# Kernel tuning notes

Measured on AMD Instinct MI355X. Metric: run time of the kernel, lower is better.

## Reference

```python
import math
import jax, jax.numpy as jnp
import numpy as np

B, N, C = 64, 197, 768
H = 12
D = C // H
SCALE = D ** -0.5
EPS_SM = 1e-6
LN_EPS = 1e-5


def _layernorm(x, w, b):
    mu = jnp.mean(x, axis=-1, keepdims=True)
    var = jnp.var(x, axis=-1, keepdims=True)
    return (x - mu) * jax.lax.rsqrt(var + LN_EPS) * w + b


def setup_inputs() -> dict:
    key = jax.random.key(0)
    ks = jax.random.split(key, 12)
    s = 0.02
    return {
        "x": jax.random.normal(ks[0], (B, N, C), jnp.float32),
        "mask": jnp.ones((B, N), jnp.float32),
        "ln1_w": jnp.ones((C,), jnp.float32),
        "ln1_b": jnp.zeros((C,), jnp.float32),
        "qkv_w": jax.random.normal(ks[1], (C, 3 * C), jnp.float32) * s,
        "qkv_b": jnp.zeros((3 * C,), jnp.float32),
        "proj_w": jax.random.normal(ks[2], (C, C), jnp.float32) * s,
        "proj_b": jnp.zeros((C,), jnp.float32),
        "ln2_w": jnp.ones((C,), jnp.float32),
        "ln2_b": jnp.zeros((C,), jnp.float32),
        "fc1_w": jax.random.normal(ks[3], (C, 4 * C), jnp.float32) * s,
        "fc1_b": jnp.zeros((4 * C,), jnp.float32),
        "fc2_w": jax.random.normal(ks[4], (4 * C, C), jnp.float32) * s,
        "fc2_b": jnp.zeros((C,), jnp.float32),
        "threshold": jnp.float32(0.0),
    }


def reference(x, mask, ln1_w, ln1_b, qkv_w, qkv_b, proj_w, proj_b,
              ln2_w, ln2_b, fc1_w, fc1_b, fc2_w, fc2_b, threshold):
    # --- LTPAttention ---
    h = _layernorm(x, ln1_w, ln1_b)
    qkv = (h @ qkv_w + qkv_b).reshape(B, N, 3, H, D)
    qkv = jnp.transpose(qkv, (2, 0, 3, 1, 4))  # (3, B, H, N, D)
    q, k, v = qkv[0], qkv[1], qkv[2]
    attn = jnp.einsum("bhnd,bhmd->bhnm", q, k) * SCALE  # (B,H,N,N)
    # softmax_with_mask (eval path): exp * key-mask, renormalize
    m = mask[:, None, None, :]  # (B,1,1,N) masks keys
    w = jnp.exp(attn - jnp.max(attn, axis=-1, keepdims=True)) * m
    attn = w / (jnp.sum(w, axis=-1, keepdims=True) + EPS_SM)
    out = jnp.einsum("bhnm,bhmd->bhnd", attn, v)
    out = jnp.transpose(out, (0, 2, 1, 3)).reshape(B, N, C)
    x_attn = out @ proj_w + proj_b
    # importance scores: mean over heads and queries -> (B, N)
    imp = jnp.mean(attn, axis=(1, 2))
    imp = imp.at[:, 0].set(jnp.inf)  # always keep CLS token
    # ThresholdMasker (eval): hard threshold
    new_mask = (imp > threshold).astype(mask.dtype)
    mask_out = jnp.where(mask > 0, new_mask, mask)
    # --- residual + MLP ---
    x = x + x_attn
    h2 = _layernorm(x, ln2_w, ln2_b)
    h2 = jax.nn.gelu(h2 @ fc1_w + fc1_b, approximate=False)
    x = x + (h2 @ fc2_w + fc2_b)
    return x, mask_out
```

## Files before the change

### kernel.cpp

```cpp
#include <hip/hip_runtime.h>
#include <hip/hip_bf16.h>
#include <math.h>

#define B_ 64
#define N_ 197
#define C_ 768
#define H_ 12
#define BN_ (B_ * N_)
#define MPAD 12672
#define GRIDM 99

typedef unsigned short ushort_t;
typedef __attribute__((ext_vector_type(8))) short short8;
typedef __attribute__((ext_vector_type(4))) float f32x4;

__device__ __forceinline__ float wave_reduce_sum(float v) {
#pragma unroll
  for (int off = 32; off; off >>= 1) v += __shfl_xor(v, off);
  return v;
}

__device__ __forceinline__ ushort_t f2bf(float f) {
  __hip_bfloat16 h = __float2bfloat16(f);
  ushort_t u;
  __builtin_memcpy(&u, &h, 2);
  return u;
}

__device__ __forceinline__ float gelu_fast(float u) {
  const float z2 = 1.5957691216f * (u + 0.044715f * u * u * u);
  const float e = __expf(z2);
  const float th = 1.f - 2.f / (e + 1.f);
  return 0.5f * u * (1.f + th);
}

__global__ __launch_bounds__(256) void wtrans_kernel(const float* __restrict__ W,
                                                     ushort_t* __restrict__ Wt,
                                                     int K, int N) {
  __shared__ ushort_t tile[32][33];
  const int bn = blockIdx.x * 32, bk = blockIdx.y * 32;
  const int tx = threadIdx.x & 31, ty = threadIdx.x >> 5;
#pragma unroll
  for (int i = ty; i < 32; i += 8)
    tile[i][tx] = f2bf(W[(size_t)(bk + i) * N + bn + tx]);
  __syncthreads();
#pragma unroll
  for (int i = ty; i < 32; i += 8)
    Wt[(size_t)(bn + i) * K + bk + tx] = tile[tx][i];
}

__global__ __launch_bounds__(256) void ln_kernel(const float* __restrict__ x,
                                                 const float* __restrict__ w,
                                                 const float* __restrict__ bsh,
                                                 ushort_t* __restrict__ out) {
  const int row = blockIdx.x;
  const float* xr = x + (size_t)row * C_;
  const int tid = threadIdx.x;
  float v0 = xr[tid], v1 = xr[tid + 256], v2 = xr[tid + 512];
  float s = v0 + v1 + v2;
  float q = v0 * v0 + v1 * v1 + v2 * v2;
  s = wave_reduce_sum(s);
  q = wave_reduce_sum(q);
  __shared__ float red[8];
  const int w4 = tid >> 6, l = tid & 63;
  if (l == 0) { red[w4] = s; red[4 + w4] = q; }
  __syncthreads();
  float ts = red[0] + red[1] + red[2] + red[3];
  float tq = red[4] + red[5] + red[6] + red[7];
  float mu = ts * (1.f / C_);
  float var = tq * (1.f / C_) - mu * mu;
  float rs = rsqrtf(var + 1e-5f);
  ushort_t* orow = out + (size_t)row * C_;
  orow[tid]       = f2bf((v0 - mu) * rs * w[tid]       + bsh[tid]);
  orow[tid + 256] = f2bf((v1 - mu) * rs * w[tid + 256] + bsh[tid + 256]);
  orow[tid + 512] = f2bf((v2 - mu) * rs * w[tid + 512] + bsh[tid + 512]);
}

template <int RES, int ACT, int OUT_BF16>
__global__ __launch_bounds__(256) void mfma_gemm(const ushort_t* __restrict__ A,
                                                 const ushort_t* __restrict__ Bt,
                                                 const float* __restrict__ bias,
                                                 const float* __restrict__ res,
                                                 void* __restrict__ Cout,
                                                 int M, int Nc, int K, int gridN) {
  __shared__ __align__(16) ushort_t As0[128][32];
  __shared__ __align__(16) ushort_t As1[128][32];
  __shared__ __align__(16) ushort_t As2[128][32];
  __shared__ __align__(16) ushort_t As3[128][32];
  __shared__ __align__(16) ushort_t Bs0[128][32];
  __shared__ __align__(16) ushort_t Bs1[128][32];
  __shared__ __align__(16) ushort_t Bs2[128][32];
  __shared__ __align__(16) ushort_t Bs3[128][32];

  const int flat = blockIdx.x;
  const int x8 = flat & 7, q8 = flat >> 3;
  const int n_t = q8 % gridN, jj = q8 / gridN;
  const int m_t = jj * 8 + x8;
  if (m_t >= GRIDM) return;

  const int tid = threadIdx.x;
  const int w = tid >> 6, l = tid & 63;
  const int bm = m_t * 128, bnn = n_t * 128;
  const int quad = l >> 4, lm = l & 15;
  const int wm = (w >> 1) * 64, wn = (w & 1) * 64;

  const int c0 = w * 2, c1 = w * 2 + 1;
  const int srow = l >> 2;
  const int scol = ((l & 3) ^ ((l >> 3) & 3)) << 3;
  const ushort_t* ag0 = A + (size_t)(bm + c0 * 16 + srow) * K + scol;
  const ushort_t* ag1 = A + (size_t)(bm + c1 * 16 + srow) * K + scol;
  const ushort_t* bg0 = Bt + (size_t)(bnn + c0 * 16 + srow) * K + scol;
  const ushort_t* bg1 = Bt + (size_t)(bnn + c1 * 16 + srow) * K + scol;

  auto stage = [&](ushort_t (*Ad)[32], ushort_t (*Bd)[32], int k0) {
    __builtin_amdgcn_global_load_lds(
        (const __attribute__((address_space(1))) void*)(ag0 + k0),
        (__attribute__((address_space(3))) void*)&Ad[c0 * 16][0], 16, 0, 0);
    __builtin_amdgcn_global_load_lds(
        (const __attribute__((address_space(1))) void*)(ag1 + k0),
        (__attribute__((address_space(3))) void*)&Ad[c1 * 16][0], 16, 0, 0);
    __builtin_amdgcn_global_load_lds(
        (const __attribute__((address_space(1))) void*)(bg0 + k0),
        (__attribute__((address_space(3))) void*)&Bd[c0 * 16][0], 16, 0, 0);
    __builtin_amdgcn_global_load_lds(
        (const __attribute__((address_space(1))) void*)(bg1 + k0),
        (__attribute__((address_space(3))) void*)&Bd[c1 * 16][0], 16, 0, 0);
  };

  const int fslot = (quad ^ ((lm >> 1) & 3)) << 3;

  f32x4 acc[4][4];
#pragma unroll
  for (int mi = 0; mi < 4; mi++)
#pragma unroll
    for (int ni = 0; ni < 4; ni++) acc[mi][ni] = (f32x4){0.f, 0.f, 0.f, 0.f};

  const int NIT = K >> 5;

#define GSTEP(Ac, Bc, An, Bn, tn, VMN, DOSTAGE)                         \
  {                                                                     \
    asm volatile("s_waitcnt vmcnt(" #VMN ")" ::: "memory");             \
    __builtin_amdgcn_s_barrier();                                       \
    asm volatile("" ::: "memory");                                      \
    if (DOSTAGE) stage(An, Bn, (tn) << 5);                              \
    short8 af[4], bf[4];                                                \
    _Pragma("unroll") for (int i = 0; i < 4; i++) {                     \
      af[i] = *(const short8*)&Ac[wm + i * 16 + lm][fslot];             \
      bf[i] = *(const short8*)&Bc[wn + i * 16 + lm][fslot];             \
    }                                                                   \
    _Pragma("unroll") for (int mi = 0; mi < 4; mi++)                    \
      _Pragma("unroll") for (int ni = 0; ni < 4; ni++)                  \
        acc[mi][ni] = __builtin_amdgcn_mfma_f32_16x16x32_bf16(          \
            af[mi], bf[ni], acc[mi][ni], 0, 0, 0);                      \
  }

  stage(As0, Bs0, 0);
  stage(As1, Bs1, 1 << 5);
  stage(As2, Bs2, 2 << 5);
  int t = 0;
  for (; t < NIT - 4; t += 4) {
    GSTEP(As0, Bs0, As3, Bs3, t + 3, 8, true);
    GSTEP(As1, Bs1, As0, Bs0, t + 4, 8, true);
    GSTEP(As2, Bs2, As1, Bs1, t + 5, 8, true);
    GSTEP(As3, Bs3, As2, Bs2, t + 6, 8, true);
  }
  GSTEP(As0, Bs0, As3, Bs3, t + 3, 8, true);
  GSTEP(As1, Bs1, As0, Bs0, 0, 8, false);
  GSTEP(As2, Bs2, As0, Bs0, 0, 4, false);
  GSTEP(As3, Bs3, As0, Bs0, 0, 0, false);
#undef GSTEP

#pragma unroll
  for (int mi = 0; mi < 4; mi++) {
#pragma unroll
    for (int ni = 0; ni < 4; ni++) {
      const int col = bnn + wn + ni * 16 + lm;
      const float bv = bias[col];
#pragma unroll
      for (int r = 0; r < 4; r++) {
        const int row = bm + wm + mi * 16 + quad * 4 + r;
        if (row < M) {
          float v = acc[mi][ni][r] + bv;
          if constexpr (RES) v += res[(size_t)row * Nc + col];
          if constexpr (ACT) v = gelu_fast(v);
          if constexpr (OUT_BF16)
            ((ushort_t*)Cout)[(size_t)row * Nc + col] = f2bf(v);
          else
            ((float*)Cout)[(size_t)row * Nc + col] = v;
        }
      }
    }
  }
}

__global__ __launch_bounds__(256, 2) void attn_mfma(const ushort_t* __restrict__ qkv,
                                                    const float* __restrict__ mask,
                                                    ushort_t* __restrict__ aout,
                                                    float* __restrict__ imp) {
  __shared__ __align__(16) ushort_t Ks[208 * 64];
  __shared__ __align__(16) ushort_t Vt[64 * 216];
  __shared__ __align__(16) ushort_t Pb[4][16 * 208];
  const int b = blockIdx.x / H_, h = blockIdx.x % H_;
  const int tid = threadIdx.x, w = tid >> 6, l = tid & 63;
  const int quad = l >> 4, lm = l & 15;
  const ushort_t* qbase = qkv + (size_t)b * N_ * 2304 + h * 64;
  const ushort_t* kbase = qbase + 768;
  const ushort_t* vbase = qbase + 1536;

  for (int idx = tid; idx < 208 * 8; idx += 256) {
    const int j = idx >> 3, g = idx & 7;
    uint4 val = make_uint4(0u, 0u, 0u, 0u);
    if (j < N_) val = *(const uint4*)(kbase + (size_t)j * 2304 + g * 8);
    *(uint4*)&Ks[j * 64 + ((g ^ (j & 7)) << 3)] = val;
  }
  for (int idx = tid; idx < 52 * 64; idx += 256) {
    const int d = idx & 63, jg = idx >> 6, j0 = jg * 4;
    ushort_t a0 = 0, a1 = 0, a2 = 0, a3 = 0;
    if (j0 + 0 < N_) a0 = vbase[(size_t)(j0 + 0) * 2304 + d];
    if (j0 + 1 < N_) a1 = vbase[(size_t)(j0 + 1) * 2304 + d];
    if (j0 + 2 < N_) a2 = vbase[(size_t)(j0 + 2) * 2304 + d];
    if (j0 + 3 < N_) a3 = vbase[(size_t)(j0 + 3) * 2304 + d];
    uint2 pk;
    pk.x = (unsigned)a0 | ((unsigned)a1 << 16);
    pk.y = (unsigned)a2 | ((unsigned)a3 << 16);
    *(uint2*)&Vt[d * 216 + j0] = pk;
  }
  float mkv[13];
#pragma unroll
  for (int t = 0; t < 13; t++) {
    const int col = t * 16 + lm;
    mkv[t] = (col < N_) ? mask[b * N_ + col] : 0.f;
  }
  float cs[13];
#pragma unroll
  for (int t = 0; t < 13; t++) cs[t] = 0.f;
  __syncthreads();

  ushort_t* pw = &Pb[w][0];
  for (int i0 = w * 16; i0 < 208; i0 += 64) {
    f32x4 accs[13];
#pragma unroll
    for (int t = 0; t < 13; t++) accs[t] = (f32x4){0.f, 0.f, 0.f, 0.f};
#pragma unroll
    for (int kh = 0; kh < 2; kh++) {
      const int k0 = kh * 32;
      const short8 aq =
          *(const short8*)(qbase + (size_t)(i0 + lm) * 2304 + k0 + quad * 8);
      const int gb = (k0 >> 3) + quad;
#pragma unroll
      for (int t = 0; t < 13; t++) {
        const int j = t * 16 + lm;
        const short8 bk = *(const short8*)&Ks[j * 64 + ((gb ^ (j & 7)) << 3)];
        accs[t] = __builtin_amdgcn_mfma_f32_16x16x32_bf16(aq, bk, accs[t], 0, 0, 0);
      }
    }
    float inv[4];
#pragma unroll
    for (int r = 0; r < 4; r++) {
      float m = -3.4e38f;
#pragma unroll
      for (int t = 0; t < 13; t++) m = fmaxf(m, accs[t][r] * 0.125f);
      m = fmaxf(m, __shfl_xor(m, 1));
      m = fmaxf(m, __shfl_xor(m, 2));
      m = fmaxf(m, __shfl_xor(m, 4));
      m = fmaxf(m, __shfl_xor(m, 8));
      float s = 0.f;
#pragma unroll
      for (int t = 0; t < 13; t++) {
        const float e = __expf(accs[t][r] * 0.125f - m) * mkv[t];
        accs[t][r] = e;
        s += e;
      }
      s += __shfl_xor(s, 1);
      s += __shfl_xor(s, 2);
      s += __shfl_xor(s, 4);
      s += __shfl_xor(s, 8);
      inv[r] = 1.f / (s + 1e-6f);
    }
    const int ibase = i0 + quad * 4;
#pragma unroll
    for (int r = 0; r < 4; r++) {
      const bool rok = (ibase + r) < N_;
#pragma unroll
      for (int t = 0; t < 13; t++) {
        const float p = accs[t][r] * inv[r];
        accs[t][r] = p;
        if (rok) cs[t] += p;
        pw[(quad * 4 + r) * 208 + t * 16 + lm] = f2bf(p);
      }
    }
    __builtin_amdgcn_wave_barrier();
    f32x4 acco[4];
#pragma unroll
    for (int n = 0; n < 4; n++) acco[n] = (f32x4){0.f, 0.f, 0.f, 0.f};
#pragma unroll
    for (int ks = 0; ks < 6; ks++) {
      const int k0 = ks * 32;
      const short8 ap = *(const short8*)&pw[lm * 208 + k0 + quad * 8];
#pragma unroll
      for (int n = 0; n < 4; n++) {
        const short8 bv = *(const short8*)&Vt[(n * 16 + lm) * 216 + k0 + quad * 8];
        acco[n] = __builtin_amdgcn_mfma_f32_16x16x32_bf16(ap, bv, acco[n], 0, 0, 0);
      }
    }
    {
      const bool lo = (quad < 2);
      short8 apt = {};
      if (lo) apt = *(const short8*)&pw[lm * 208 + 192 + quad * 8];
#pragma unroll
      for (int n = 0; n < 4; n++) {
        short8 bvt = {};
        if (lo) bvt = *(const short8*)&Vt[(n * 16 + lm) * 216 + 192 + quad * 8];
        acco[n] = __builtin_amdgcn_mfma_f32_16x16x32_bf16(apt, bvt, acco[n], 0, 0, 0);
      }
    }
#pragma unroll
    for (int r = 0; r < 4; r++) {
      const int i = ibase + r;
      if (i < N_) {
#pragma unroll
        for (int n = 0; n < 4; n++)
          aout[(size_t)(b * N_ + i) * C_ + h * 64 + n * 16 + lm] = f2bf(acco[n][r]);
      }
    }
  }
#pragma unroll
  for (int t = 0; t < 13; t++) {
    float v = cs[t];
    v += __shfl_xor(v, 16);
    v += __shfl_xor(v, 32);
    if (l < 16) {
      const int col = t * 16 + l;
      if (col < N_)
        atomicAdd(&imp[b * N_ + col], v * (1.f / (H_ * (float)N_)));
    }
  }
}

__global__ __launch_bounds__(256) void mask_kernel(const float* __restrict__ imp,
                                                   const float* __restrict__ mask,
                                                   const float* __restrict__ thr,
                                                   float* __restrict__ mask_out) {
  const int i = blockIdx.x * 256 + threadIdx.x;
  if (i >= BN_) return;
  const int n = i % N_;
  const float iv = (n == 0) ? INFINITY : imp[i];
  const float m = mask[i];
  const float nm = (iv > thr[0]) ? 1.f : 0.f;
  mask_out[i] = (m > 0.f) ? nm : m;
}

extern "C" void kernel_launch(void* const* d_in, const int* in_sizes, int n_in,
                              void* d_out, int out_size, void* d_ws, size_t ws_size,
                              hipStream_t stream) {
  const float* x      = (const float*)d_in[0];
  const float* mask   = (const float*)d_in[1];
  const float* ln1_w  = (const float*)d_in[2];
  const float* ln1_b  = (const float*)d_in[3];
  const float* qkv_w  = (const float*)d_in[4];
  const float* qkv_b  = (const float*)d_in[5];
  const float* proj_w = (const float*)d_in[6];
  const float* proj_b = (const float*)d_in[7];
  const float* ln2_w  = (const float*)d_in[8];
  const float* ln2_b  = (const float*)d_in[9];
  const float* fc1_w  = (const float*)d_in[10];
  const float* fc1_b  = (const float*)d_in[11];
  const float* fc2_w  = (const float*)d_in[12];
  const float* fc2_b  = (const float*)d_in[13];
  const float* thr    = (const float*)d_in[14];

  float* out = (float*)d_out;
  float* mask_out = out + (size_t)BN_ * C_;

  ushort_t* buf0    = (ushort_t*)d_ws;
  ushort_t* hbuf    = buf0 + (size_t)MPAD * 3072;
  ushort_t* aoutb   = hbuf + (size_t)MPAD * 768;
  ushort_t* qkv_wt  = aoutb + (size_t)MPAD * 768;
  ushort_t* proj_wt = qkv_wt + (size_t)2304 * 768;
  ushort_t* fc1_wt  = proj_wt + (size_t)768 * 768;
  ushort_t* fc2_wt  = fc1_wt + (size_t)3072 * 768;
  float*    impb    = (float*)(fc2_wt + (size_t)768 * 3072);

  hipMemsetAsync(impb, 0, BN_ * sizeof(float), stream);

  wtrans_kernel<<<dim3(2304 / 32, 768 / 32), 256, 0, stream>>>(qkv_w, qkv_wt, 768, 2304);
  wtrans_kernel<<<dim3(768 / 32, 768 / 32), 256, 0, stream>>>(proj_w, proj_wt, 768, 768);
  wtrans_kernel<<<dim3(3072 / 32, 768 / 32), 256, 0, stream>>>(fc1_w, fc1_wt, 768, 3072);
  wtrans_kernel<<<dim3(768 / 32, 3072 / 32), 256, 0, stream>>>(fc2_w, fc2_wt, 3072, 768);

  const int MS = 13 * 8;
  ln_kernel<<<BN_, 256, 0, stream>>>(x, ln1_w, ln1_b, hbuf);
  mfma_gemm<0, 0, 1><<<MS * 18, 256, 0, stream>>>(
      hbuf, qkv_wt, qkv_b, nullptr, buf0, BN_, 2304, 768, 18);
  attn_mfma<<<B_ * H_, 256, 0, stream>>>(buf0, mask, aoutb, impb);
  mask_kernel<<<(BN_ + 255) / 256, 256, 0, stream>>>(impb, mask, thr, mask_out);
  mfma_gemm<1, 0, 0><<<MS * 6, 256, 0, stream>>>(
      aoutb, proj_wt, proj_b, x, out, BN_, 768, 768, 6);
  ln_kernel<<<BN_, 256, 0, stream>>>(out, ln2_w, ln2_b, hbuf);
  mfma_gemm<0, 1, 1><<<MS * 24, 256, 0, stream>>>(
      hbuf, fc1_wt, fc1_b, nullptr, buf0, BN_, 3072, 768, 24);
  mfma_gemm<1, 0, 0><<<MS * 6, 256, 0, stream>>>(
      buf0, fc2_wt, fc2_b, out, out, BN_, 768, 3072, 6);
}
```

Measured before the change: 603.3 us.

## Replace four-stage BK=32 GEMM ring with double-buffered BK=64 pipeline

Restructures the MFMA GEMM main loop from a four-slot ring of 32-wide K tiles, which uses fine-grained vmcnt waits, into a two-buffer scheme. Each buffer holds a 64-wide K tile split into two 32-column halves, and full __syncthreads separate the stages. The aim is fewer barriers per K element and simpler control flow. In exchange, prefetch depth drops to one tile ahead and each barrier waits for all outstanding loads, so memory latency may be hidden less well. The loop also assumes K/64 is even.

```diff
diff --git a/kernel.cpp b/kernel.cpp
--- a/kernel.cpp
+++ b/kernel.cpp
@@ -83,14 +83,14 @@
                                                  const float* __restrict__ res,
                                                  void* __restrict__ Cout,
                                                  int M, int Nc, int K, int gridN) {
-  __shared__ __align__(16) ushort_t As0[128][32];
-  __shared__ __align__(16) ushort_t As1[128][32];
-  __shared__ __align__(16) ushort_t As2[128][32];
-  __shared__ __align__(16) ushort_t As3[128][32];
-  __shared__ __align__(16) ushort_t Bs0[128][32];
-  __shared__ __align__(16) ushort_t Bs1[128][32];
-  __shared__ __align__(16) ushort_t Bs2[128][32];
-  __shared__ __align__(16) ushort_t Bs3[128][32];
+  __shared__ __align__(16) ushort_t As0h0[128][32];
+  __shared__ __align__(16) ushort_t As0h1[128][32];
+  __shared__ __align__(16) ushort_t As1h0[128][32];
+  __shared__ __align__(16) ushort_t As1h1[128][32];
+  __shared__ __align__(16) ushort_t Bs0h0[128][32];
+  __shared__ __align__(16) ushort_t Bs0h1[128][32];
+  __shared__ __align__(16) ushort_t Bs1h0[128][32];
+  __shared__ __align__(16) ushort_t Bs1h1[128][32];
 
   const int flat = blockIdx.x;
   const int x8 = flat & 7, q8 = flat >> 3;
@@ -112,7 +112,7 @@
   const ushort_t* bg0 = Bt + (size_t)(bnn + c0 * 16 + srow) * K + scol;
   const ushort_t* bg1 = Bt + (size_t)(bnn + c1 * 16 + srow) * K + scol;
 
-  auto stage = [&](ushort_t (*Ad)[32], ushort_t (*Bd)[32], int k0) {
+  auto stage_h = [&](ushort_t (*Ad)[32], ushort_t (*Bd)[32], int k0) {
     __builtin_amdgcn_global_load_lds(
         (const __attribute__((address_space(1))) void*)(ag0 + k0),
         (__attribute__((address_space(3))) void*)&Ad[c0 * 16][0], 16, 0, 0);
@@ -135,14 +135,8 @@
 #pragma unroll
     for (int ni = 0; ni < 4; ni++) acc[mi][ni] = (f32x4){0.f, 0.f, 0.f, 0.f};
 
-  const int NIT = K >> 5;
-
-#define GSTEP(Ac, Bc, An, Bn, tn, VMN, DOSTAGE)                         \
+#define KHALF(Ac, Bc)                                                   \
   {                                                                     \
-    asm volatile("s_waitcnt vmcnt(" #VMN ")" ::: "memory");             \
-    __builtin_amdgcn_s_barrier();                                       \
-    asm volatile("" ::: "memory");                                      \
-    if (DOSTAGE) stage(An, Bn, (tn) << 5);                              \
     short8 af[4], bf[4];                                                \
     _Pragma("unroll") for (int i = 0; i < 4; i++) {                     \
       af[i] = *(const short8*)&Ac[wm + i * 16 + lm][fslot];             \
@@ -154,21 +148,27 @@
             af[mi], bf[ni], acc[mi][ni], 0, 0, 0);                      \
   }
 
-  stage(As0, Bs0, 0);
-  stage(As1, Bs1, 1 << 5);
-  stage(As2, Bs2, 2 << 5);
-  int t = 0;
-  for (; t < NIT - 4; t += 4) {
-    GSTEP(As0, Bs0, As3, Bs3, t + 3, 8, true);
-    GSTEP(As1, Bs1, As0, Bs0, t + 4, 8, true);
-    GSTEP(As2, Bs2, As1, Bs1, t + 5, 8, true);
-    GSTEP(As3, Bs3, As2, Bs2, t + 6, 8, true);
-  }
-  GSTEP(As0, Bs0, As3, Bs3, t + 3, 8, true);
-  GSTEP(As1, Bs1, As0, Bs0, 0, 8, false);
-  GSTEP(As2, Bs2, As0, Bs0, 0, 4, false);
-  GSTEP(As3, Bs3, As0, Bs0, 0, 0, false);
-#undef GSTEP
+  const int NIT = K >> 6;
+
+  stage_h(As0h0, Bs0h0, 0);
+  stage_h(As0h1, Bs0h1, 32);
+  for (int t = 0; t < NIT; t += 2) {
+    __syncthreads();
+    if (t + 1 < NIT) {
+      stage_h(As1h0, Bs1h0, (t + 1) * 64);
+      stage_h(As1h1, Bs1h1, (t + 1) * 64 + 32);
+    }
+    KHALF(As0h0, Bs0h0);
+    KHALF(As0h1, Bs0h1);
+    __syncthreads();
+    if (t + 2 < NIT) {
+      stage_h(As0h0, Bs0h0, (t + 2) * 64);
+      stage_h(As0h1, Bs0h1, (t + 2) * 64 + 32);
+    }
+    KHALF(As1h0, Bs1h0);
+    KHALF(As1h1, Bs1h1);
+  }
+#undef KHALF
 
 #pragma unroll
   for (int mi = 0; mi < 4; mi++) {
```

New measurement: 621.3 us. 1.03x slower.
